# Performance work log

Hardware: AMD Instinct MI355X
Metric: run time of the kernel (lower is better)

Reference implementation:

```python
import jax, jax.numpy as jnp
import numpy as np

K = 56          # kernel_size (attended axis length)
HEADS = 8
IN_C = 64
OUT_C = 64
DH = OUT_C // HEADS  # 8; q,k use DH//2=4 channels, v uses DH=8
F_QR = 0.1
F_KR = 0.1
F_SVE = 0.1
F_SV = 1.0
EPS = 1e-5


def _bn(x, g, b, axes):
    # batch-norm in training mode: batch statistics over `axes`, affine per channel dim 1
    m = jnp.mean(x, axes, keepdims=True)
    v = jnp.var(x, axes, keepdims=True)
    shp = [1] * x.ndim
    shp[1] = -1
    return (x - m) * jax.lax.rsqrt(v + EPS) * g.reshape(shp) + b.reshape(shp)


def setup_inputs() -> dict:
    key = jax.random.key(0)
    ks = jax.random.split(key, 3)
    x = jax.random.normal(ks[0], (1, IN_C, 32, 56, K), dtype=jnp.float32)
    w_qkv = jax.random.normal(ks[1], (2 * OUT_C, IN_C), dtype=jnp.float32) * np.sqrt(1.0 / IN_C)
    relative = jax.random.normal(ks[2], (2 * DH, 2 * K - 1), dtype=jnp.float32) * np.sqrt(1.0 / DH)
    return {
        "x": x,
        "w_qkv": w_qkv,
        "relative": relative,
        "bn_qkv_g": jnp.ones((2 * OUT_C,), jnp.float32),
        "bn_qkv_b": jnp.zeros((2 * OUT_C,), jnp.float32),
        "bn_sim_g": jnp.ones((3 * HEADS,), jnp.float32),
        "bn_sim_b": jnp.zeros((3 * HEADS,), jnp.float32),
        "bn_out_g": jnp.ones((2 * OUT_C,), jnp.float32),
        "bn_out_b": jnp.zeros((2 * OUT_C,), jnp.float32),
    }


def reference(x, w_qkv, relative, bn_qkv_g, bn_qkv_b, bn_sim_g, bn_sim_b, bn_out_g, bn_out_b):
    N, C, D, Hdim, Wdim = x.shape  # axial='width': attend over W == K
    xp = jnp.transpose(x, (0, 2, 3, 1, 4)).reshape(N * D * Hdim, C, Wdim)  # (B, C, K)
    # 1x1 conv1d (no bias) + BN1d
    qkv = jnp.einsum("bci,oc->boi", xp, w_qkv)
    qkv = _bn(qkv, bn_qkv_g, bn_qkv_b, (0, 2))
    qkv = qkv.reshape(-1, HEADS, 2 * DH, K)
    q = qkv[:, :, : DH // 2]
    k = qkv[:, :, DH // 2 : DH]
    v = qkv[:, :, DH:]
    # relative position embeddings: emb[c,i,j] = relative[c, i - j + K - 1]
    idx = jnp.arange(K)
    rel_idx = idx[:, None] - idx[None, :] + K - 1  # (K, K)
    emb = relative[:, rel_idx]  # (2*DH, K, K)
    q_e, k_e, v_e = emb[: DH // 2], emb[DH // 2 : DH], emb[DH:]
    qr = jnp.einsum("bgci,cij->bgij", q, q_e) * F_QR
    kr = jnp.transpose(jnp.einsum("bgci,cij->bgij", k, k_e), (0, 1, 3, 2)) * F_KR
    qk = jnp.einsum("bgci,bgcj->bgij", q, k)
    stacked = jnp.concatenate([qk, qr, kr], axis=1)  # (B, 3*heads, K, K)
    stacked = _bn(stacked, bn_sim_g, bn_sim_b, (0, 2, 3))
    sim = jax.nn.softmax(stacked.reshape(-1, 3, HEADS, K, K).sum(axis=1), axis=3)
    sv = jnp.einsum("bgij,bgcj->bgci", sim, v) * F_SV
    sve = jnp.einsum("bgij,cij->bgci", sim, v_e) * F_SVE
    so = jnp.concatenate([sv, sve], axis=-1).reshape(-1, 2 * OUT_C, K)
    so = _bn(so, bn_out_g, bn_out_b, (0, 2))
    out = so.reshape(N, D, Hdim, OUT_C, 2, K).sum(axis=4)
    return jnp.transpose(out, (0, 3, 1, 2, 4))  # back to (N, OUT_C, D, H, W)
```

## Files before the change

kernel.cpp:

```cpp
#include <hip/hip_runtime.h>
#include <math.h>

typedef float v2f __attribute__((ext_vector_type(2)));

constexpr int KW      = 56;
constexpr int NB      = 1792;
constexpr int QKV_CH  = 128;
constexpr int SIM_CH  = 24;
constexpr int SLOTS   = 64;
constexpr int SMASK   = 63;
constexpr float EPS   = 1e-5f;

constexpr int   PA[10]  = {0,0,0,0,1,1,1,2,2,3};
constexpr int   PB[10]  = {0,1,2,3,1,2,3,2,3,3};
constexpr float PMf[10] = {1,2,2,2,1,2,2,1,2,1};

#if __has_builtin(__builtin_amdgcn_exp2f)
#define EXP2(x) __builtin_amdgcn_exp2f(x)
#else
#define EXP2(x) __expf((x) * 0.6931471805599453f)
#endif

__global__ __launch_bounds__(256) void k_qkv(const float* __restrict__ x,
                                             const float* __restrict__ w,
                                             const float* __restrict__ rel,
                                             float* __restrict__ qkv,
                                             float* __restrict__ sums,
                                             float* __restrict__ tabs) {
    const int t = threadIdx.x;
    if (blockIdx.x >= NB) {
        const int t0 = (blockIdx.x - NB) * 256 + t;
        const int STR = 8 * 256;
        float* Rq  = tabs;
        float* Rk  = tabs + 224;
        float* E2q = tabs + 448;
        float* E2k = tabs + 1008;
        float4* TQF = (float4*)(tabs + 1568);
        float4* TVF = (float4*)(tabs + 2464);
        for (int idx = t0; idx < 448; idx += STR) {
            int which = idx / 224, r = idx % 224;
            int i = r >> 2, c = r & 3;
            const float* src = rel + (which * 4 + c) * 111;
            float s = 0.f;
            for (int tt = 0; tt < 56; ++tt) s += src[i + tt];
            (which ? Rk : Rq)[r] = s;
        }
        for (int idx = t0; idx < 1120; idx += STR) {
            int which = idx / 560, r = idx % 560;
            int i = r / 10, p = r % 10;
            const float* sa = rel + (which * 4 + PA[p]) * 111;
            const float* sb = rel + (which * 4 + PB[p]) * 111;
            float s = 0.f;
            for (int tt = 0; tt < 56; ++tt) s += sa[i + tt] * sb[i + tt];
            (which ? E2k : E2q)[r] = s;
        }
        for (int d = t0; d < 112; d += STR) {
            bool v = d < 111;
            float4 tq, tk, ta, tb;
            tq.x = v ? rel[0 * 111 + d] : 0.f;
            tq.y = v ? rel[1 * 111 + d] : 0.f;
            tq.z = v ? rel[2 * 111 + d] : 0.f;
            tq.w = v ? rel[3 * 111 + d] : 0.f;
            tk.x = v ? rel[4 * 111 + 110 - d] : 0.f;
            tk.y = v ? rel[5 * 111 + 110 - d] : 0.f;
            tk.z = v ? rel[6 * 111 + 110 - d] : 0.f;
            tk.w = v ? rel[7 * 111 + 110 - d] : 0.f;
            ta.x = v ? rel[8 * 111 + d] : 0.f;
            ta.y = v ? rel[9 * 111 + d] : 0.f;
            ta.z = v ? rel[10 * 111 + d] : 0.f;
            ta.w = v ? rel[11 * 111 + d] : 0.f;
            tb.x = v ? rel[12 * 111 + d] : 0.f;
            tb.y = v ? rel[13 * 111 + d] : 0.f;
            tb.z = v ? rel[14 * 111 + d] : 0.f;
            tb.w = v ? rel[15 * 111 + d] : 0.f;
            TQF[d]       = tq;
            TQF[112 + d] = tk;
            TVF[d]       = ta;
            TVF[112 + d] = tb;
        }
        return;
    }
    __shared__ float xs[64 * KW];
    __shared__ float wt[64 * 128];
    __shared__ float s1[128], s2[128];
    const int b = blockIdx.x;

    if (t < 128) { s1[t] = 0.f; s2[t] = 0.f; }
    for (int idx = t; idx < 896; idx += 256) {
        int c = idx / 14, r = idx % 14;
        float4 v = *(const float4*)&x[c * 100352 + b * 56 + r * 4];
        *(float4*)&xs[c * 56 + r * 4] = v;
    }
    for (int idx = t; idx < 2048; idx += 256) {
        int o = idx >> 4, cq = idx & 15;
        float4 v = *(const float4*)&w[o * 64 + cq * 4];
        wt[(cq * 4 + 0) * 128 + o] = v.x;
        wt[(cq * 4 + 1) * 128 + o] = v.y;
        wt[(cq * 4 + 2) * 128 + o] = v.z;
        wt[(cq * 4 + 3) * 128 + o] = v.w;
    }
    __syncthreads();

    if (t < 224) {
        const int ob = t & 31, ib = t >> 5;
        v2f acc[4][4];
#pragma unroll
        for (int o = 0; o < 4; ++o)
#pragma unroll
            for (int ip = 0; ip < 4; ++ip) acc[o][ip] = (v2f)(0.f);
        for (int c = 0; c < 64; ++c) {
            float4 wv = *(const float4*)&wt[c * 128 + (ob << 2)];
            float4 x0 = *(const float4*)&xs[c * 56 + (ib << 3)];
            float4 x1 = *(const float4*)&xs[c * 56 + (ib << 3) + 4];
            v2f xp[4];
            xp[0] = (v2f){x0.x, x0.y}; xp[1] = (v2f){x0.z, x0.w};
            xp[2] = (v2f){x1.x, x1.y}; xp[3] = (v2f){x1.z, x1.w};
            v2f wd[4];
            wd[0] = (v2f)(wv.x); wd[1] = (v2f)(wv.y);
            wd[2] = (v2f)(wv.z); wd[3] = (v2f)(wv.w);
#pragma unroll
            for (int o = 0; o < 4; ++o)
#pragma unroll
                for (int ip = 0; ip < 4; ++ip)
                    acc[o][ip] += wd[o] * xp[ip];
        }
#pragma unroll
        for (int i = 0; i < 8; ++i) {
            float4 st;
            st.x = acc[0][i >> 1][i & 1];
            st.y = acc[1][i >> 1][i & 1];
            st.z = acc[2][i >> 1][i & 1];
            st.w = acc[3][i >> 1][i & 1];
            *(float4*)&qkv[b * 7168 + (ib * 8 + i) * 128 + ob * 4] = st;
        }
#pragma unroll
        for (int o = 0; o < 4; ++o) {
            float ps = 0.f, ps2 = 0.f;
#pragma unroll
            for (int ip = 0; ip < 4; ++ip) {
                ps  += acc[o][ip].x + acc[o][ip].y;
                ps2 += acc[o][ip].x * acc[o][ip].x + acc[o][ip].y * acc[o][ip].y;
            }
            atomicAdd(&s1[ob * 4 + o], ps);
            atomicAdd(&s2[ob * 4 + o], ps2);
        }
    }
    __syncthreads();
    if (t < 128) {
        float* dst = sums + (b & SMASK) * 256;
        atomicAdd(&dst[t], s1[t]);
        atomicAdd(&dst[128 + t], s2[t]);
    }
}

__global__ void k_coef(const float* __restrict__ sums, const float* __restrict__ g,
                       const float* __restrict__ bb, float* __restrict__ coef,
                       int nch, float invM) {
    const int o = blockIdx.x;
    const int s = threadIdx.x;
    float a1 = sums[s * 2 * nch + o];
    float a2 = sums[s * 2 * nch + nch + o];
#pragma unroll
    for (int mk = 1; mk < 64; mk <<= 1) {
        a1 += __shfl_xor(a1, mk);
        a2 += __shfl_xor(a2, mk);
    }
    if (s == 0) {
        float mean = a1 * invM;
        float var  = fmaxf(a2 * invM - mean * mean, 0.f);
        float sc   = g[o] * rsqrtf(var + EPS);
        coef[o] = sc;
        coef[nch + o] = bb[o] - mean * sc;
    }
}

__global__ __launch_bounds__(256) void k_simstats(const float* __restrict__ qkv,
                                                  const float* __restrict__ qcoef,
                                                  const float* __restrict__ Rq,
                                                  const float* __restrict__ Rk,
                                                  const float* __restrict__ E2q,
                                                  const float* __restrict__ E2k,
                                                  float* __restrict__ ssum) {
    const int wid = threadIdx.x >> 6, lane = threadIdx.x & 63;
    const int unit = blockIdx.x * 4 + wid;
    const int b = unit >> 3, g = unit & 7;
    const int iL = lane < 56 ? lane : 55;
    const float valid = lane < 56 ? 1.f : 0.f;

    const float* row = qkv + b * 7168 + iL * 128 + g * 16;
    float4 q4 = *(const float4*)(row);
    float4 k4 = *(const float4*)(row + 4);
    const float4 aq = *(const float4*)&qcoef[g * 16];
    const float4 ak = *(const float4*)&qcoef[g * 16 + 4];
    const float4 cq = *(const float4*)&qcoef[QKV_CH + g * 16];
    const float4 ck = *(const float4*)&qcoef[QKV_CH + g * 16 + 4];
    float qv[4], kv[4];
    qv[0] = (q4.x * aq.x + cq.x) * valid;
    qv[1] = (q4.y * aq.y + cq.y) * valid;
    qv[2] = (q4.z * aq.z + cq.z) * valid;
    qv[3] = (q4.w * aq.w + cq.w) * valid;
    kv[0] = (k4.x * ak.x + ck.x) * valid;
    kv[1] = (k4.y * ak.y + ck.y) * valid;
    kv[2] = (k4.z * ak.z + ck.z) * valid;
    kv[3] = (k4.w * ak.w + ck.w) * valid;

    float4 rq = *(const float4*)&Rq[iL * 4];
    float4 rk = *(const float4*)&Rk[iL * 4];
    float e2q[10], e2k[10];
#pragma unroll
    for (int p = 0; p < 10; ++p) { e2q[p] = E2q[iL * 10 + p]; e2k[p] = E2k[iL * 10 + p]; }

    float red[32];
#pragma unroll
    for (int c = 0; c < 4; ++c) { red[c] = qv[c]; red[4 + c] = kv[c]; }
#pragma unroll
    for (int p = 0; p < 10; ++p) {
        red[8 + p]  = qv[PA[p]] * qv[PB[p]];
        red[18 + p] = kv[PA[p]] * kv[PB[p]];
    }
    {
        float rqa[4] = {rq.x, rq.y, rq.z, rq.w};
        float rka[4] = {rk.x, rk.y, rk.z, rk.w};
        float pq = 0.f, pk = 0.f, pq2 = 0.f, pk2 = 0.f;
#pragma unroll
        for (int c = 0; c < 4; ++c) { pq += qv[c] * rqa[c]; pk += kv[c] * rka[c]; }
#pragma unroll
        for (int p = 0; p < 10; ++p) {
            pq2 += PMf[p] * red[8 + p]  * e2q[p];
            pk2 += PMf[p] * red[18 + p] * e2k[p];
        }
        red[28] = pq; red[29] = pk; red[30] = pq2; red[31] = pk2;
    }
#pragma unroll
    for (int v = 0; v < 32; ++v) {
        float xv = red[v];
#pragma unroll
        for (int mk = 1; mk < 64; mk <<= 1) xv += __shfl_xor(xv, mk);
        red[v] = xv;
    }
    float sqk = 0.f, sqk2 = 0.f;
#pragma unroll
    for (int c = 0; c < 4; ++c) sqk += red[c] * red[4 + c];
#pragma unroll
    for (int p = 0; p < 10; ++p) sqk2 += PMf[p] * red[8 + p] * red[18 + p];
    if (lane == 0) {
        float* ss = ssum + (blockIdx.x & SMASK) * 48;
        atomicAdd(&ss[g], sqk);
        atomicAdd(&ss[8 + g], 0.1f * red[28]);
        atomicAdd(&ss[16 + g], 0.1f * red[29]);
        atomicAdd(&ss[SIM_CH + g], sqk2);
        atomicAdd(&ss[SIM_CH + 8 + g], 0.01f * red[30]);
        atomicAdd(&ss[SIM_CH + 16 + g], 0.01f * red[31]);
    }
}

__global__ __launch_bounds__(256) void k_attn(const float* __restrict__ qkv,
                                              const float* __restrict__ qcoef,
                                              const float* __restrict__ scoef,
                                              const float4* __restrict__ TQF,
                                              const float4* __restrict__ TVF,
                                              float* __restrict__ sv2,
                                              float* __restrict__ sve2,
                                              float* __restrict__ osums) {
    __shared__ float4 TQs[224];
    __shared__ float4 TVs[224];
    __shared__ float4 KVs[4 * 168];
    __shared__ float Lsum[128];
    const int t = threadIdx.x;
    const int wid = t >> 6, lane = t & 63;
    const int unit = blockIdx.x * 4 + wid;
    const int b = unit >> 3, g = unit & 7;
    const int iL = lane < 56 ? lane : 55;

    if (t < 224) { TQs[t] = TQF[t]; TVs[t] = TVF[t]; }

    const float* row = qkv + b * 7168 + iL * 128 + g * 16;
    float4 q4  = *(const float4*)(row);
    float4 k4  = *(const float4*)(row + 4);
    float4 va4 = *(const float4*)(row + 8);
    float4 vb4 = *(const float4*)(row + 12);
    const float4 a0 = *(const float4*)&qcoef[g * 16];
    const float4 a1 = *(const float4*)&qcoef[g * 16 + 4];
    const float4 a2 = *(const float4*)&qcoef[g * 16 + 8];
    const float4 a3 = *(const float4*)&qcoef[g * 16 + 12];
    const float4 c0 = *(const float4*)&qcoef[QKV_CH + g * 16];
    const float4 c1 = *(const float4*)&qcoef[QKV_CH + g * 16 + 4];
    const float4 c2 = *(const float4*)&qcoef[QKV_CH + g * 16 + 8];
    const float4 c3 = *(const float4*)&qcoef[QKV_CH + g * 16 + 12];
    float4 kh, vh, wh;
    kh.x = k4.x * a1.x + c1.x;  kh.y = k4.y * a1.y + c1.y;
    kh.z = k4.z * a1.z + c1.z;  kh.w = k4.w * a1.w + c1.w;
    vh.x = va4.x * a2.x + c2.x; vh.y = va4.y * a2.y + c2.y;
    vh.z = va4.z * a2.z + c2.z; vh.w = va4.w * a2.w + c2.w;
    wh.x = vb4.x * a3.x + c3.x; wh.y = vb4.y * a3.y + c3.y;
    wh.z = vb4.z * a3.z + c3.z; wh.w = vb4.w * a3.w + c3.w;
    float qh[4];
    qh[0] = q4.x * a0.x + c0.x;  qh[1] = q4.y * a0.y + c0.y;
    qh[2] = q4.z * a0.z + c0.z;  qh[3] = q4.w * a0.w + c0.w;

    KVs[wid * 168 + iL]       = kh;
    KVs[wid * 168 + 56 + iL]  = vh;
    KVs[wid * 168 + 112 + iL] = wh;
    __syncthreads();

    const float L2E = 1.44269504088896340736f;
    const float aqk = scoef[g] * L2E;
    const float aqr = scoef[8 + g] * 0.1f * L2E;
    const float akr = scoef[16 + g] * 0.1f * L2E;
    const float cc2 = (scoef[SIM_CH + g] + scoef[SIM_CH + 8 + g]
                       + scoef[SIM_CH + 16 + g]) * L2E;
    const v2f qa01 = {qh[0] * aqk, qh[1] * aqk};
    const v2f qa23 = {qh[2] * aqk, qh[3] * aqk};
    const v2f qr01 = {qh[0] * aqr, qh[1] * aqr};
    const v2f qr23 = {qh[2] * aqr, qh[3] * aqr};
    const v2f akrp = {akr, akr};

    float l = 0.f;
    v2f sva = (v2f)(0.f), svb = (v2f)(0.f), svc = (v2f)(0.f), svd = (v2f)(0.f);
    v2f sea = (v2f)(0.f), seb = (v2f)(0.f), sec = (v2f)(0.f), sed = (v2f)(0.f);

    const float4* tqp = TQs + 55 + iL;
    const float4* tvp = TVs + 55 + iL;
    const float4* kvp = KVs + wid * 168;

#pragma unroll 4
    for (int j = 0; j < 56; ++j) {
        float4 tq = tqp[-j];
        float4 tk = tqp[112 - j];
        float4 ta = tvp[-j];
        float4 tb = tvp[112 - j];
        float4 kj = kvp[j];
        float4 vj = kvp[56 + j];
        float4 wj = kvp[112 + j];
        v2f u01 = akrp * (v2f){tk.x, tk.y} + qa01;
        v2f u23 = akrp * (v2f){tk.z, tk.w} + qa23;
        v2f acc = u01 * (v2f){kj.x, kj.y};
        acc += u23 * (v2f){kj.z, kj.w};
        acc += qr01 * (v2f){tq.x, tq.y};
        acc += qr23 * (v2f){tq.z, tq.w};
        float e = EXP2(acc.x + acc.y + cc2);
        l += e;
        v2f ep = {e, e};
        sva += ep * (v2f){vj.x, vj.y};
        svb += ep * (v2f){vj.z, vj.w};
        svc += ep * (v2f){wj.x, wj.y};
        svd += ep * (v2f){wj.z, wj.w};
        sea += ep * (v2f){ta.x, ta.y};
        seb += ep * (v2f){ta.z, ta.w};
        sec += ep * (v2f){tb.x, tb.y};
        sed += ep * (v2f){tb.z, tb.w};
    }
    const float inv = 1.f / l;
    const float inv1 = 0.1f * inv;
    float osv[8], ose[8];
    osv[0] = sva.x * inv;  osv[1] = sva.y * inv;
    osv[2] = svb.x * inv;  osv[3] = svb.y * inv;
    osv[4] = svc.x * inv;  osv[5] = svc.y * inv;
    osv[6] = svd.x * inv;  osv[7] = svd.y * inv;
    ose[0] = sea.x * inv1; ose[1] = sea.y * inv1;
    ose[2] = seb.x * inv1; ose[3] = seb.y * inv1;
    ose[4] = sec.x * inv1; ose[5] = sec.y * inv1;
    ose[6] = sed.x * inv1; ose[7] = sed.y * inv1;

    if (lane < 56) {
        size_t base = ((size_t)(g * 8) * 1792 + b) * 56 + iL;
#pragma unroll
        for (int c = 0; c < 8; ++c) {
            sv2[base + (size_t)c * 100352]  = osv[c];
            sve2[base + (size_t)c * 100352] = ose[c];
        }
    }
    const float valid = lane < 56 ? 1.f : 0.f;
    float red[32];
#pragma unroll
    for (int c = 0; c < 8; ++c) {
        red[c]      = osv[c] * valid;
        red[8 + c]  = ose[c] * valid;
        red[16 + c] = osv[c] * osv[c] * valid;
        red[24 + c] = ose[c] * ose[c] * valid;
    }
#pragma unroll
    for (int v = 0; v < 32; ++v) {
        float xv = red[v];
#pragma unroll
        for (int mk = 1; mk < 64; mk <<= 1) xv += __shfl_xor(xv, mk);
        red[v] = xv;
    }
    if (lane == 0) {
#pragma unroll
        for (int v = 0; v < 32; ++v) Lsum[wid * 32 + v] = red[v];
    }
    __syncthreads();
    if (t < 128) {
        const int ws_ = t >> 5, v = t & 31;
        const int g_ = (blockIdx.x * 4 + ws_) & 7;
        const int addr = ((v >> 4) & 1) * 128 + g_ * 16 + 2 * (v & 7) + ((v >> 3) & 1);
        float* dst = osums + (blockIdx.x & SMASK) * 256;
        atomicAdd(&dst[addr], Lsum[t]);
    }
}

__global__ __launch_bounds__(256) void k_out(const float* __restrict__ sv2,
                                             const float* __restrict__ sve2,
                                             const float* __restrict__ ocoef,
                                             float* __restrict__ out) {
    int e4 = blockIdx.x * 256 + threadIdx.x;
    int i0 = e4 * 4;
    int oc = i0 / 100352;
    int o0 = 2 * oc;
    float A = ocoef[o0], B = ocoef[o0 + 1];
    float C = ocoef[QKV_CH + o0] + ocoef[QKV_CH + o0 + 1];
    float4 v0 = *(const float4*)&sv2[i0];
    float4 v1 = *(const float4*)&sve2[i0];
    float4 r;
    r.x = A * v0.x + B * v1.x + C;
    r.y = A * v0.y + B * v1.y + C;
    r.z = A * v0.z + B * v1.z + C;
    r.w = A * v0.w + B * v1.w + C;
    *(float4*)&out[i0] = r;
}

extern "C" void kernel_launch(void* const* d_in, const int* in_sizes, int n_in,
                              void* d_out, int out_size, void* d_ws, size_t ws_size,
                              hipStream_t stream) {
    const float* x     = (const float*)d_in[0];
    const float* wqkv  = (const float*)d_in[1];
    const float* rel   = (const float*)d_in[2];
    const float* g_qkv = (const float*)d_in[3];
    const float* b_qkv = (const float*)d_in[4];
    const float* g_sim = (const float*)d_in[5];
    const float* b_sim = (const float*)d_in[6];
    const float* g_out = (const float*)d_in[7];
    const float* b_out = (const float*)d_in[8];
    float* out = (float*)d_out;
    float* ws = (float*)d_ws;

    float* qkv_raw  = ws;
    float* sv2      = ws + 12845056;
    float* sve2     = ws + 19267584;
    float* stats    = ws + 25690112;
    float* sums_buf = stats;
    float* qkv_coef = stats + 16384;
    float* sim_coef = stats + 16640;
    float* out_coef = stats + 16688;
    float* tabs     = stats + 16944;
    float* Rq   = tabs;
    float* Rk   = tabs + 224;
    float* E2q  = tabs + 448;
    float* E2k  = tabs + 1008;
    float4* TQF = (float4*)(tabs + 1568);
    float4* TVF = (float4*)(tabs + 2464);

    hipMemsetAsync(sums_buf, 0, SLOTS * 256 * sizeof(float), stream);

    k_qkv<<<NB + 8, 256, 0, stream>>>(x, wqkv, rel, qkv_raw, sums_buf, tabs);
    k_coef<<<QKV_CH, 64, 0, stream>>>(sums_buf, g_qkv, b_qkv, qkv_coef, QKV_CH,
                                      1.0f / 100352.0f);
    hipMemsetAsync(sums_buf, 0, SLOTS * 48 * sizeof(float), stream);
    k_simstats<<<3584, 256, 0, stream>>>(qkv_raw, qkv_coef, Rq, Rk, E2q, E2k,
                                         sums_buf);
    k_coef<<<SIM_CH, 64, 0, stream>>>(sums_buf, g_sim, b_sim, sim_coef, SIM_CH,
                                      1.0f / 5619712.0f);
    hipMemsetAsync(sums_buf, 0, SLOTS * 256 * sizeof(float), stream);
    k_attn<<<3584, 256, 0, stream>>>(qkv_raw, qkv_coef, sim_coef, TQF, TVF,
                                     sv2, sve2, sums_buf);
    k_coef<<<QKV_CH, 64, 0, stream>>>(sums_buf, g_out, b_out, out_coef, QKV_CH,
                                      1.0f / 100352.0f);
    k_out<<<6272, 256, 0, stream>>>(sv2, sve2, out_coef, out);
}
```

Baseline: 266.6 us.

## Use halving butterfly reductions and pad weight tile to avoid bank conflicts

Replaces the per-value full 64-lane shuffle reductions in k_simstats and k_attn with a recursive-halving butterfly, where each step exchanges half the remaining values. This cuts shuffle count from 32x6 to 31+1, leaving one partial result per lane that is mapped back through a bit-reversed index. k_attn now issues its atomics directly from lanes, dropping the shared-memory staging and block barrier. Separately, the weight tile in k_qkv is padded to a row stride of 132 to reduce LDS bank conflicts on the transposed stores.

```diff
diff --git a/kernel.cpp b/kernel.cpp
--- a/kernel.cpp
+++ b/kernel.cpp
@@ -81,7 +81,7 @@
         return;
     }
     __shared__ float xs[64 * KW];
-    __shared__ float wt[64 * 128];
+    __shared__ float wt[64 * 132];
     __shared__ float s1[128], s2[128];
     const int b = blockIdx.x;
 
@@ -94,10 +94,10 @@
     for (int idx = t; idx < 2048; idx += 256) {
         int o = idx >> 4, cq = idx & 15;
         float4 v = *(const float4*)&w[o * 64 + cq * 4];
-        wt[(cq * 4 + 0) * 128 + o] = v.x;
-        wt[(cq * 4 + 1) * 128 + o] = v.y;
-        wt[(cq * 4 + 2) * 128 + o] = v.z;
-        wt[(cq * 4 + 3) * 128 + o] = v.w;
+        wt[(cq * 4 + 0) * 132 + o] = v.x;
+        wt[(cq * 4 + 1) * 132 + o] = v.y;
+        wt[(cq * 4 + 2) * 132 + o] = v.z;
+        wt[(cq * 4 + 3) * 132 + o] = v.w;
     }
     __syncthreads();
 
@@ -109,7 +109,7 @@
 #pragma unroll
             for (int ip = 0; ip < 4; ++ip) acc[o][ip] = (v2f)(0.f);
         for (int c = 0; c < 64; ++c) {
-            float4 wv = *(const float4*)&wt[c * 128 + (ob << 2)];
+            float4 wv = *(const float4*)&wt[c * 132 + (ob << 2)];
             float4 x0 = *(const float4*)&xs[c * 56 + (ib << 3)];
             float4 x1 = *(const float4*)&xs[c * 56 + (ib << 3) + 4];
             v2f xp[4];
@@ -181,6 +181,7 @@
                                                   const float* __restrict__ E2q,
                                                   const float* __restrict__ E2k,
                                                   float* __restrict__ ssum) {
+    __shared__ float Sst[4][32];
     const int wid = threadIdx.x >> 6, lane = threadIdx.x & 63;
     const int unit = blockIdx.x * 4 + wid;
     const int b = unit >> 3, g = unit & 7;
@@ -221,36 +222,51 @@
     {
         float rqa[4] = {rq.x, rq.y, rq.z, rq.w};
         float rka[4] = {rk.x, rk.y, rk.z, rk.w};
-        float pq = 0.f, pk = 0.f, pq2 = 0.f, pk2 = 0.f;
+        float pq = 0.f, pk = 0.f, pq2 = 0.f, pk2_ = 0.f;
 #pragma unroll
         for (int c = 0; c < 4; ++c) { pq += qv[c] * rqa[c]; pk += kv[c] * rka[c]; }
 #pragma unroll
         for (int p = 0; p < 10; ++p) {
             pq2 += PMf[p] * red[8 + p]  * e2q[p];
-            pk2 += PMf[p] * red[18 + p] * e2k[p];
-        }
-        red[28] = pq; red[29] = pk; red[30] = pq2; red[31] = pk2;
-    }
-#pragma unroll
-    for (int v = 0; v < 32; ++v) {
-        float xv = red[v];
-#pragma unroll
-        for (int mk = 1; mk < 64; mk <<= 1) xv += __shfl_xor(xv, mk);
-        red[v] = xv;
-    }
-    float sqk = 0.f, sqk2 = 0.f;
-#pragma unroll
-    for (int c = 0; c < 4; ++c) sqk += red[c] * red[4 + c];
-#pragma unroll
-    for (int p = 0; p < 10; ++p) sqk2 += PMf[p] * red[8 + p] * red[18 + p];
+            pk2_ += PMf[p] * red[18 + p] * e2k[p];
+        }
+        red[28] = pq; red[29] = pk; red[30] = pq2; red[31] = pk2_;
+    }
+#pragma unroll
+    for (int k = 0; k < 5; ++k) {
+        const int m = 1 << k;
+        const int half = 16 >> k;
+        const bool up = (lane & m) != 0;
+#pragma unroll
+        for (int v = 0; v < half; ++v) {
+            float a = up ? red[v + half] : red[v];
+            float bsend = up ? red[v] : red[v + half];
+            red[v] = a + __shfl_xor(bsend, m);
+        }
+    }
+    red[0] += __shfl_xor(red[0], 32);
+    const int vIdx = ((lane & 1) << 4) | ((lane & 2) << 2) | (lane & 4)
+                   | ((lane & 8) >> 2) | ((lane & 16) >> 4);
+    if (lane < 32) Sst[wid][vIdx] = red[0];
+    __syncthreads();
     if (lane == 0) {
+        float S[32];
+#pragma unroll
+        for (int q = 0; q < 8; ++q) {
+            float4 f = *(const float4*)&Sst[wid][q * 4];
+            S[q * 4] = f.x; S[q * 4 + 1] = f.y; S[q * 4 + 2] = f.z; S[q * 4 + 3] = f.w;
+        }
+        float sqk = S[0] * S[4] + S[1] * S[5] + S[2] * S[6] + S[3] * S[7];
+        float sqk2 = 0.f;
+#pragma unroll
+        for (int p = 0; p < 10; ++p) sqk2 += PMf[p] * S[8 + p] * S[18 + p];
         float* ss = ssum + (blockIdx.x & SMASK) * 48;
         atomicAdd(&ss[g], sqk);
-        atomicAdd(&ss[8 + g], 0.1f * red[28]);
-        atomicAdd(&ss[16 + g], 0.1f * red[29]);
+        atomicAdd(&ss[8 + g], 0.1f * S[28]);
+        atomicAdd(&ss[16 + g], 0.1f * S[29]);
         atomicAdd(&ss[SIM_CH + g], sqk2);
-        atomicAdd(&ss[SIM_CH + 8 + g], 0.01f * red[30]);
-        atomicAdd(&ss[SIM_CH + 16 + g], 0.01f * red[31]);
+        atomicAdd(&ss[SIM_CH + 8 + g], 0.01f * S[30]);
+        atomicAdd(&ss[SIM_CH + 16 + g], 0.01f * S[31]);
     }
 }
 
@@ -265,7 +281,6 @@
     __shared__ float4 TQs[224];
     __shared__ float4 TVs[224];
     __shared__ float4 KVs[4 * 168];
-    __shared__ float Lsum[128];
     const int t = threadIdx.x;
     const int wid = t >> 6, lane = t & 63;
     const int unit = blockIdx.x * 4 + wid;
@@ -380,23 +395,24 @@
         red[24 + c] = ose[c] * ose[c] * valid;
     }
 #pragma unroll
-    for (int v = 0; v < 32; ++v) {
-        float xv = red[v];
-#pragma unroll
-        for (int mk = 1; mk < 64; mk <<= 1) xv += __shfl_xor(xv, mk);
-        red[v] = xv;
-    }
-    if (lane == 0) {
-#pragma unroll
-        for (int v = 0; v < 32; ++v) Lsum[wid * 32 + v] = red[v];
-    }
-    __syncthreads();
-    if (t < 128) {
-        const int ws_ = t >> 5, v = t & 31;
-        const int g_ = (blockIdx.x * 4 + ws_) & 7;
-        const int addr = ((v >> 4) & 1) * 128 + g_ * 16 + 2 * (v & 7) + ((v >> 3) & 1);
+    for (int k = 0; k < 5; ++k) {
+        const int m = 1 << k;
+        const int half = 16 >> k;
+        const bool up = (lane & m) != 0;
+#pragma unroll
+        for (int v = 0; v < half; ++v) {
+            float a = up ? red[v + half] : red[v];
+            float bsend = up ? red[v] : red[v + half];
+            red[v] = a + __shfl_xor(bsend, m);
+        }
+    }
+    red[0] += __shfl_xor(red[0], 32);
+    if (lane < 32) {
+        const int v = ((lane & 1) << 4) | ((lane & 2) << 2) | (lane & 4)
+                    | ((lane & 8) >> 2) | ((lane & 16) >> 4);
+        const int addr = ((v >> 4) & 1) * 128 + g * 16 + 2 * (v & 7) + ((v >> 3) & 1);
         float* dst = osums + (blockIdx.x & SMASK) * 256;
-        atomicAdd(&dst[addr], Lsum[t]);
+        atomicAdd(&dst[addr], red[0]);
     }
 }
 
```

After: 370.5 us. +39.0%, slower.
